# Optimization experiments

Measured on AMD Instinct MI355X. Metric: run time of the kernel, lower is better.

The kernel has to match this reference:

```python
import jax, jax.numpy as jnp
import numpy as np

N_NODES = 50000
N_EDGES = 800000
IN_DIM, HID_DIM, OUT_DIM = 128, 128, 64


def setup_inputs() -> dict:
    key = jax.random.key(0)
    ks = jax.random.split(key, 8)
    x = jax.random.normal(ks[0], (N_NODES, IN_DIM), dtype=jnp.float32)
    edge_index = jax.random.randint(ks[1], (2, N_EDGES), 0, N_NODES, dtype=jnp.int64)
    # GCNConv uses Glorot weights + zero bias; any random init is fine for a reference
    W1 = jax.random.normal(ks[2], (IN_DIM, HID_DIM), dtype=jnp.float32) / np.sqrt(IN_DIM)
    b1 = jnp.zeros((HID_DIM,), dtype=jnp.float32)
    W2 = jax.random.normal(ks[3], (HID_DIM, OUT_DIM), dtype=jnp.float32) / np.sqrt(HID_DIM)
    b2 = jnp.zeros((OUT_DIM,), dtype=jnp.float32)
    Wfc = jax.random.normal(ks[4], (OUT_DIM, 2), dtype=jnp.float32) / np.sqrt(OUT_DIM)
    bfc = jnp.zeros((2,), dtype=jnp.float32)
    return {"x": x, "edge_index": edge_index, "W1": W1, "b1": b1,
            "W2": W2, "b2": b2, "Wfc": Wfc, "bfc": bfc}


def _gcn_conv(x, src, dst, W, b, n_nodes):
    """PyG GCNConv: out = D^{-1/2} (A+I) D^{-1/2} (x W) + b."""
    xw = x @ W  # [N, F_out] transform before propagation
    ones = jnp.ones(src.shape[0], dtype=xw.dtype)
    deg = jax.ops.segment_sum(ones, dst, num_segments=n_nodes) + 1.0  # +1 for self-loop
    dinv = jax.lax.rsqrt(deg)
    norm = dinv[src] * dinv[dst]  # [E]
    msg = xw[src] * norm[:, None]  # gather + scale: [E, F_out]
    agg = jax.ops.segment_sum(msg, dst, num_segments=n_nodes)  # scatter-add
    agg = agg + xw * (dinv * dinv)[:, None]  # self-loop contribution (norm = 1/deg)
    return agg + b


def reference(x, edge_index, W1, b1, W2, b2, Wfc, bfc):
    n = x.shape[0]
    src, dst = edge_index[0], edge_index[1]
    h = jax.nn.relu(_gcn_conv(x, src, dst, W1, b1, n))
    # dropout is identity in eval mode
    h = _gcn_conv(h, src, dst, W2, b2, n)
    h = h @ Wfc + bfc
    return jax.nn.leaky_relu(h, negative_slope=0.01)
```

## Files before the change

kernel.cpp:

```cpp
#include <hip/hip_runtime.h>
#include <hip/hip_fp16.h>

#define IN_DIM 128
#define HID_DIM 128
#define OUT_DIM 64
#define BINW 128
#define BINSHIFT 7
#define MAXBIN 512
#define CAP 4096
#define CNTSTRIDE 16

__global__ __launch_bounds__(256) void k_scatter(const int* __restrict__ src,
                                                 const int* __restrict__ dst,
                                                 int* __restrict__ bin_cnt,
                                                 int* __restrict__ ovf_cnt,
                                                 unsigned int* __restrict__ ovf,
                                                 unsigned int* __restrict__ ebin,
                                                 int E, int nbin) {
    __shared__ int h[MAXBIN];
    __shared__ int base_s[MAXBIN];
    int t = threadIdx.x;
    for (int k = t; k < nbin; k += 256) h[k] = 0;
    __syncthreads();
    int per = E / gridDim.x;
    int ebeg = blockIdx.x * per;
    int eend = (blockIdx.x + 1 == gridDim.x) ? E : ebeg + per;
    for (int i = ebeg + t; i < eend; i += 256)
        atomicAdd(&h[dst[i] >> BINSHIFT], 1);
    __syncthreads();
    for (int k = t; k < nbin; k += 256) {
        int c = h[k];
        base_s[k] = (c > 0) ? atomicAdd(&bin_cnt[k * CNTSTRIDE], c) : 0;
        h[k] = 0;
    }
    __syncthreads();
    for (int i = ebeg + t; i < eend; i += 256) {
        unsigned int s = (unsigned int)src[i];
        unsigned int d = (unsigned int)dst[i];
        int b = (int)(d >> BINSHIFT);
        int pos = base_s[b] + atomicAdd(&h[b], 1);
        unsigned int packed = s | (d << 16);
        if (pos < CAP) ebin[(size_t)b * CAP + pos] = packed;
        else ovf[atomicAdd(ovf_cnt, 1)] = packed;
    }
}

__global__ __launch_bounds__(256) void k_fill(const unsigned int* __restrict__ ebin,
                                              const int* __restrict__ bin_cnt,
                                              const int* __restrict__ ovf_cnt,
                                              const unsigned int* __restrict__ ovf,
                                              int* __restrict__ row_ptr,
                                              unsigned short* __restrict__ degu,
                                              unsigned short* __restrict__ csr_src,
                                              float* __restrict__ dinv,
                                              const float* __restrict__ W2,
                                              const float* __restrict__ Wfc,
                                              const float* __restrict__ b2,
                                              const float* __restrict__ bfc,
                                              float* __restrict__ Wc,
                                              float* __restrict__ bc,
                                              int N, int nbin) {
    __shared__ int cnt[BINW];
    __shared__ int excl[BINW];
    __shared__ int start[BINW];
    int k = blockIdx.x;
    int node0 = k * BINW;
    int nn = min(BINW, N - node0);
    int t = threadIdx.x;
    if (t < BINW) cnt[t] = 0;
    __syncthreads();
    int cnt_k = min(bin_cnt[k * CNTSTRIDE], CAP);
    const unsigned int* seg = ebin + (size_t)k * CAP;
    for (int i = t; i < cnt_k; i += 256)
        atomicAdd(&cnt[(seg[i] >> 16) & (BINW - 1)], 1);
    int novf = *ovf_cnt;
    for (int i = t; i < novf; i += 256) {
        unsigned int e = ovf[i];
        if ((int)(e >> (16 + BINSHIFT)) == k)
            atomicAdd(&cnt[(e >> 16) & (BINW - 1)], 1);
    }
    __syncthreads();
    if (t < BINW) excl[t] = (t < nn) ? cnt[t] : 0;
    __syncthreads();
    for (int off = 1; off < BINW; off <<= 1) {
        int u = 0;
        if (t < BINW && t >= off) u = excl[t - off];
        __syncthreads();
        if (t < BINW) excl[t] += u;
        __syncthreads();
    }
    if (t < nn) {
        int deg = cnt[t];
        int e0 = k * CAP + excl[t] - deg;
        start[t] = e0;
        row_ptr[node0 + t] = e0;
        degu[node0 + t] = (unsigned short)deg;
        dinv[node0 + t] = rsqrtf((float)deg + 1.0f);
        cnt[t] = 0;
    }
    __syncthreads();
    for (int i = t; i < cnt_k; i += 256) {
        unsigned int e = seg[i];
        int dl = (e >> 16) & (BINW - 1);
        int slot = start[dl] + atomicAdd(&cnt[dl], 1);
        csr_src[slot] = (unsigned short)(e & 0xffffu);
    }
    for (int i = t; i < novf; i += 256) {
        unsigned int e = ovf[i];
        if ((int)(e >> (16 + BINSHIFT)) == k) {
            int dl = (e >> 16) & (BINW - 1);
            int slot = start[dl] + atomicAdd(&cnt[dl], 1);
            csr_src[slot] = (unsigned short)(e & 0xffffu);
        }
    }
    if (k == 0) {
        int kk = t >> 1, j = t & 1;
        float acc = 0.f;
#pragma unroll 8
        for (int m = 0; m < OUT_DIM; ++m) acc += W2[kk * OUT_DIM + m] * Wfc[m * 2 + j];
        Wc[kk * 2 + j] = acc;
        if (kk == 0) {
            float b = 0.f;
#pragma unroll 8
            for (int m = 0; m < OUT_DIM; ++m) b += b2[m] * Wfc[m * 2 + j];
            bc[j] = b + bfc[j];
        }
    }
}

__global__ __launch_bounds__(256) void k_gemm1(const float* __restrict__ x,
                                               const float* __restrict__ W,
                                               const float* __restrict__ dinv,
                                               __half* __restrict__ xwh, int N) {
    __shared__ float Ws[64][128];
    int tid = threadIdx.x;
    float4* Ws4 = (float4*)&Ws[0][0];
    int tx = tid & 15, ty = tid >> 4;
    int row0 = blockIdx.x * 128;
    int rows[8];
    const float* xr[8];
#pragma unroll
    for (int j = 0; j < 8; ++j) {
        int row = row0 + ty + 16 * j;
        rows[j] = row;
        if (row > N - 1) row = N - 1;
        xr[j] = x + (size_t)row * IN_DIM;
    }
    float4 aclo[8], achi[8];
#pragma unroll
    for (int j = 0; j < 8; ++j) {
        aclo[j] = make_float4(0.f, 0.f, 0.f, 0.f);
        achi[j] = make_float4(0.f, 0.f, 0.f, 0.f);
    }
#pragma unroll
    for (int ph = 0; ph < 2; ++ph) {
        const float4* W4 = (const float4*)(W + (size_t)ph * 64 * HID_DIM);
#pragma unroll
        for (int i = 0; i < 8; ++i) Ws4[tid + 256 * i] = W4[tid + 256 * i];
        __syncthreads();
#pragma unroll 2
        for (int k4 = 0; k4 < 16; ++k4) {
            float4 av[8];
#pragma unroll
            for (int j = 0; j < 8; ++j) av[j] = *(const float4*)(xr[j] + ph * 64 + k4 * 4);
#pragma unroll
            for (int kk = 0; kk < 4; ++kk) {
                float4 blo = *(const float4*)&Ws[k4 * 4 + kk][4 * tx];
                float4 bhi = *(const float4*)&Ws[k4 * 4 + kk][64 + 4 * tx];
#pragma unroll
                for (int j = 0; j < 8; ++j) {
                    float a = (kk == 0) ? av[j].x : (kk == 1) ? av[j].y : (kk == 2) ? av[j].z : av[j].w;
                    aclo[j].x += a * blo.x; aclo[j].y += a * blo.y;
                    aclo[j].z += a * blo.z; aclo[j].w += a * blo.w;
                    achi[j].x += a * bhi.x; achi[j].y += a * bhi.y;
                    achi[j].z += a * bhi.z; achi[j].w += a * bhi.w;
                }
            }
        }
        __syncthreads();
    }
#pragma unroll
    for (int j = 0; j < 8; ++j) {
        if (rows[j] < N) {
            float dd = dinv[rows[j]];
            union { __half2 h[2]; uint2 u; } lo, hi;
            lo.h[0] = __floats2half2_rn(aclo[j].x * dd, aclo[j].y * dd);
            lo.h[1] = __floats2half2_rn(aclo[j].z * dd, aclo[j].w * dd);
            hi.h[0] = __floats2half2_rn(achi[j].x * dd, achi[j].y * dd);
            hi.h[1] = __floats2half2_rn(achi[j].z * dd, achi[j].w * dd);
            uint2* p = (uint2*)(xwh + (size_t)rows[j] * HID_DIM);
            p[tx] = lo.u;
            p[16 + tx] = hi.u;
        }
    }
}

__global__ __launch_bounds__(256) void k_agg1z(const int* __restrict__ row_ptr,
                                               const unsigned short* __restrict__ degu,
                                               const unsigned short* __restrict__ csr_src,
                                               const float* __restrict__ dinv,
                                               const __half* __restrict__ xwh,
                                               const float* __restrict__ b1,
                                               const float* __restrict__ Wc,
                                               float* __restrict__ z, int N) {
    constexpr int F = HID_DIM;
    constexpr int L = F / 8;
    constexpr int EPW = 64 / L;
    __shared__ float Wcs[HID_DIM * 2];
    int tid = threadIdx.x;
    if (tid < 64) ((float4*)Wcs)[tid] = ((const float4*)Wc)[tid];
    __syncthreads();
    int node = (blockIdx.x * 256 + tid) >> 6;
    if (node >= N) return;
    int lane = tid & 63;
    int sub = lane / L;
    int c   = lane % L;
    int beg = row_ptr[node];
    int end = beg + degu[node];
    float dd = dinv[node];
    uint4 us = *(const uint4*)(xwh + (size_t)node * F + c * 8);
    float4 b1a = *(const float4*)(b1 + c * 8);
    float4 b1b = *(const float4*)(b1 + c * 8 + 4);
    float a0 = 0.f, a1 = 0.f, a2 = 0.f, a3 = 0.f;
    float a4 = 0.f, a5 = 0.f, a6 = 0.f, a7 = 0.f;
    auto acc = [&](uint4 u) {
        float2 v0 = __half22float2(*(__half2*)&u.x);
        float2 v1 = __half22float2(*(__half2*)&u.y);
        float2 v2 = __half22float2(*(__half2*)&u.z);
        float2 v3 = __half22float2(*(__half2*)&u.w);
        a0 += v0.x; a1 += v0.y; a2 += v1.x; a3 += v1.y;
        a4 += v2.x; a5 += v2.y; a6 += v3.x; a7 += v3.y;
    };
    int j = beg + sub;
    for (; j + 3 * EPW < end; j += 4 * EPW) {
        int s0 = csr_src[j];
        int s1 = csr_src[j + EPW];
        int s2 = csr_src[j + 2 * EPW];
        int s3 = csr_src[j + 3 * EPW];
        uint4 u0 = *(const uint4*)(xwh + (size_t)s0 * F + c * 8);
        uint4 u1 = *(const uint4*)(xwh + (size_t)s1 * F + c * 8);
        uint4 u2 = *(const uint4*)(xwh + (size_t)s2 * F + c * 8);
        uint4 u3 = *(const uint4*)(xwh + (size_t)s3 * F + c * 8);
        acc(u0); acc(u1); acc(u2); acc(u3);
    }
    for (; j < end; j += EPW) {
        int s = csr_src[j];
        acc(*(const uint4*)(xwh + (size_t)s * F + c * 8));
    }
#pragma unroll
    for (int off = L; off < 64; off <<= 1) {
        a0 += __shfl_xor(a0, off); a1 += __shfl_xor(a1, off);
        a2 += __shfl_xor(a2, off); a3 += __shfl_xor(a3, off);
        a4 += __shfl_xor(a4, off); a5 += __shfl_xor(a5, off);
        a6 += __shfl_xor(a6, off); a7 += __shfl_xor(a7, off);
    }
    float2 v0 = __half22float2(*(__half2*)&us.x);
    float2 v1 = __half22float2(*(__half2*)&us.y);
    float2 v2 = __half22float2(*(__half2*)&us.z);
    float2 v3 = __half22float2(*(__half2*)&us.w);
    float h[8];
    h[0] = fmaxf((a0 + v0.x) * dd + b1a.x, 0.f);
    h[1] = fmaxf((a1 + v0.y) * dd + b1a.y, 0.f);
    h[2] = fmaxf((a2 + v1.x) * dd + b1a.z, 0.f);
    h[3] = fmaxf((a3 + v1.y) * dd + b1a.w, 0.f);
    h[4] = fmaxf((a4 + v2.x) * dd + b1b.x, 0.f);
    h[5] = fmaxf((a5 + v2.y) * dd + b1b.y, 0.f);
    h[6] = fmaxf((a6 + v3.x) * dd + b1b.z, 0.f);
    h[7] = fmaxf((a7 + v3.y) * dd + b1b.w, 0.f);
    float o0 = 0.f, o1 = 0.f;
#pragma unroll
    for (int k = 0; k < 8; ++k) {
        o0 += h[k] * Wcs[(c * 8 + k) * 2 + 0];
        o1 += h[k] * Wcs[(c * 8 + k) * 2 + 1];
    }
#pragma unroll
    for (int off = 1; off < L; off <<= 1) {
        o0 += __shfl_xor(o0, off);
        o1 += __shfl_xor(o1, off);
    }
    if (lane == 0) {
        float2 r; r.x = o0 * dd; r.y = o1 * dd;
        *(float2*)(z + (size_t)node * 2) = r;
    }
}

__global__ __launch_bounds__(256) void k_agg2(const int* __restrict__ row_ptr,
                                              const unsigned short* __restrict__ degu,
                                              const unsigned short* __restrict__ csr_src,
                                              const float* __restrict__ dinv,
                                              const float* __restrict__ z,
                                              const float* __restrict__ bc,
                                              float* __restrict__ out, int N) {
    int tid = threadIdx.x;
    int gwave = (blockIdx.x * 256 + tid) >> 6;
    int lane = tid & 63;
    int grp = lane >> 3, li = lane & 7;
    int node = gwave * 8 + grp;
    if (node >= N) return;
    int beg = row_ptr[node];
    int end = beg + degu[node];
    float s0 = 0.f, s1 = 0.f;
    int j = beg + li;
    for (; j + 8 < end; j += 16) {
        int sa = csr_src[j];
        int sb = csr_src[j + 8];
        float2 za = *(const float2*)(z + (size_t)sa * 2);
        float2 zb = *(const float2*)(z + (size_t)sb * 2);
        s0 += za.x + zb.x; s1 += za.y + zb.y;
    }
    if (j < end) {
        int s = csr_src[j];
        float2 zv = *(const float2*)(z + (size_t)s * 2);
        s0 += zv.x; s1 += zv.y;
    }
#pragma unroll
    for (int off = 1; off < 8; off <<= 1) {
        s0 += __shfl_xor(s0, off);
        s1 += __shfl_xor(s1, off);
    }
    if (li == 0) {
        float2 zs = *(const float2*)(z + (size_t)node * 2);
        float dd = dinv[node];
        float o0 = (s0 + zs.x) * dd + bc[0];
        float o1 = (s1 + zs.y) * dd + bc[1];
        float2 r;
        r.x = o0 > 0.f ? o0 : 0.01f * o0;
        r.y = o1 > 0.f ? o1 : 0.01f * o1;
        *(float2*)(out + (size_t)node * 2) = r;
    }
}

extern "C" void kernel_launch(void* const* d_in, const int* in_sizes, int n_in,
                              void* d_out, int out_size, void* d_ws, size_t ws_size,
                              hipStream_t stream) {
    const float* x   = (const float*)d_in[0];
    const int*   ei  = (const int*)d_in[1];
    const float* W1  = (const float*)d_in[2];
    const float* b1  = (const float*)d_in[3];
    const float* W2  = (const float*)d_in[4];
    const float* b2  = (const float*)d_in[5];
    const float* Wfc = (const float*)d_in[6];
    const float* bfc = (const float*)d_in[7];

    const int N = in_sizes[0] / IN_DIM;
    const int E = in_sizes[1] / 2;
    const int* src = ei;
    const int* dst = ei + E;
    const int nbin = (N + BINW - 1) / BINW;

    char* base = (char*)d_ws;
    size_t off = 0;
    auto take = [&](size_t bytes) { size_t o = off; off = (off + bytes + 255) & ~(size_t)255; return (void*)(base + o); };
    int*    row_ptr  = (int*)take((size_t)N * 4);
    unsigned short* degu = (unsigned short*)take((size_t)N * 2);
    unsigned short* csr_src = (unsigned short*)take((size_t)nbin * CAP * 2);
    int*    bin_cnt  = (int*)take((size_t)(nbin * CNTSTRIDE + CNTSTRIDE) * 4);
    int*    ovf_cnt  = bin_cnt + nbin * CNTSTRIDE;
    unsigned int* ovf = (unsigned int*)take((size_t)E * 4);
    unsigned int* ebin = (unsigned int*)take((size_t)nbin * CAP * 4);
    float*  dinv     = (float*)take((size_t)N * 4);
    __half* xw1h     = (__half*)take((size_t)N * HID_DIM * 2);
    float*  zbuf     = (float*)take((size_t)N * 2 * 4);
    float*  Wc       = (float*)take((size_t)HID_DIM * 2 * 4);
    float*  bc       = (float*)take(2 * 4);

    hipMemsetAsync(bin_cnt, 0, (size_t)(nbin * CNTSTRIDE + CNTSTRIDE) * 4, stream);

    k_scatter<<<256, 256, 0, stream>>>(src, dst, bin_cnt, ovf_cnt, ovf, ebin, E, nbin);
    k_fill<<<nbin, 256, 0, stream>>>(ebin, bin_cnt, ovf_cnt, ovf, row_ptr, degu,
                                     csr_src, dinv, W2, Wfc, b2, bfc, Wc, bc, N, nbin);

    const int nTile = (N + 127) / 128;

    k_gemm1<<<nTile, 256, 0, stream>>>(x, W1, dinv, xw1h, N);
    k_agg1z<<<(N + 3) / 4, 256, 0, stream>>>(row_ptr, degu, csr_src, dinv, xw1h, b1, Wc, zbuf, N);
    const int nAgg2 = ((N + 7) / 8 * 64 + 255) / 256;
    k_agg2<<<nAgg2, 256, 0, stream>>>(row_ptr, degu, csr_src, dinv, zbuf, bc, (float*)d_out, N);
}
```

Measured before the change: 178.1 us.

## Split layer-1 aggregation into four 32-feature passes with slab layout

The GEMM now writes the half-precision hidden features as four column slabs of 32 features (each N x 32) instead of one row-major N x 128 array. The aggregation kernel runs one pass per slab, so each gather touches 64-byte rows and the working set of each pass (about 3.2 MB) fits in cache, with the four passes running as separate block ranges. The partial projections are summed and scaled by dinv in a new small kernel. In exchange, the CSR edge lists are read four times and there is an extra launch plus a partial-result buffer.

```diff
diff --git a/kernel.cpp b/kernel.cpp
--- a/kernel.cpp
+++ b/kernel.cpp
@@ -9,6 +9,8 @@
 #define MAXBIN 512
 #define CAP 4096
 #define CNTSTRIDE 16
+#define PDIM 32
+#define NPASS (HID_DIM / PDIM)
 
 __global__ __launch_bounds__(256) void k_scatter(const int* __restrict__ src,
                                                  const int* __restrict__ dst,
@@ -131,7 +133,7 @@
 __global__ __launch_bounds__(256) void k_gemm1(const float* __restrict__ x,
                                                const float* __restrict__ W,
                                                const float* __restrict__ dinv,
-                                               __half* __restrict__ xwh, int N) {
+                                               __half* __restrict__ xwp, int N) {
     __shared__ float Ws[64][128];
     int tid = threadIdx.x;
     float4* Ws4 = (float4*)&Ws[0][0];
@@ -179,6 +181,7 @@
         }
         __syncthreads();
     }
+    int plo = tx >> 3, c32 = 4 * (tx & 7);
 #pragma unroll
     for (int j = 0; j < 8; ++j) {
         if (rows[j] < N) {
@@ -188,39 +191,40 @@
             lo.h[1] = __floats2half2_rn(aclo[j].z * dd, aclo[j].w * dd);
             hi.h[0] = __floats2half2_rn(achi[j].x * dd, achi[j].y * dd);
             hi.h[1] = __floats2half2_rn(achi[j].z * dd, achi[j].w * dd);
-            uint2* p = (uint2*)(xwh + (size_t)rows[j] * HID_DIM);
-            p[tx] = lo.u;
-            p[16 + tx] = hi.u;
+            *(uint2*)(xwp + ((size_t)plo * N + rows[j]) * PDIM + c32) = lo.u;
+            *(uint2*)(xwp + ((size_t)(plo + 2) * N + rows[j]) * PDIM + c32) = hi.u;
         }
     }
 }
 
-__global__ __launch_bounds__(256) void k_agg1z(const int* __restrict__ row_ptr,
-                                               const unsigned short* __restrict__ degu,
-                                               const unsigned short* __restrict__ csr_src,
-                                               const float* __restrict__ dinv,
-                                               const __half* __restrict__ xwh,
-                                               const float* __restrict__ b1,
-                                               const float* __restrict__ Wc,
-                                               float* __restrict__ z, int N) {
-    constexpr int F = HID_DIM;
-    constexpr int L = F / 8;
-    constexpr int EPW = 64 / L;
+__global__ __launch_bounds__(256) void k_agg1zp(const int* __restrict__ row_ptr,
+                                                const unsigned short* __restrict__ degu,
+                                                const unsigned short* __restrict__ csr_src,
+                                                const float* __restrict__ dinv,
+                                                const __half* __restrict__ xwp,
+                                                const float* __restrict__ b1,
+                                                const float* __restrict__ Wc,
+                                                float* __restrict__ zp,
+                                                int N, int nodeBlocks) {
     __shared__ float Wcs[HID_DIM * 2];
     int tid = threadIdx.x;
     if (tid < 64) ((float4*)Wcs)[tid] = ((const float4*)Wc)[tid];
     __syncthreads();
-    int node = (blockIdx.x * 256 + tid) >> 6;
+    int pass = blockIdx.x / nodeBlocks;
+    int nb   = blockIdx.x % nodeBlocks;
+    int node = nb * 4 + (tid >> 6);
     if (node >= N) return;
     int lane = tid & 63;
-    int sub = lane / L;
-    int c   = lane % L;
+    int sub = lane >> 2;
+    int c   = lane & 3;
     int beg = row_ptr[node];
     int end = beg + degu[node];
+    const __half* xp = xwp + (size_t)pass * N * PDIM;
     float dd = dinv[node];
-    uint4 us = *(const uint4*)(xwh + (size_t)node * F + c * 8);
-    float4 b1a = *(const float4*)(b1 + c * 8);
-    float4 b1b = *(const float4*)(b1 + c * 8 + 4);
+    uint4 us = *(const uint4*)(xp + (size_t)node * PDIM + c * 8);
+    int d0 = pass * PDIM + c * 8;
+    float4 b1a = *(const float4*)(b1 + d0);
+    float4 b1b = *(const float4*)(b1 + d0 + 4);
     float a0 = 0.f, a1 = 0.f, a2 = 0.f, a3 = 0.f;
     float a4 = 0.f, a5 = 0.f, a6 = 0.f, a7 = 0.f;
     auto acc = [&](uint4 u) {
@@ -232,23 +236,19 @@
         a4 += v2.x; a5 += v2.y; a6 += v3.x; a7 += v3.y;
     };
     int j = beg + sub;
-    for (; j + 3 * EPW < end; j += 4 * EPW) {
+    for (; j + 16 < end; j += 32) {
         int s0 = csr_src[j];
-        int s1 = csr_src[j + EPW];
-        int s2 = csr_src[j + 2 * EPW];
-        int s3 = csr_src[j + 3 * EPW];
-        uint4 u0 = *(const uint4*)(xwh + (size_t)s0 * F + c * 8);
-        uint4 u1 = *(const uint4*)(xwh + (size_t)s1 * F + c * 8);
-        uint4 u2 = *(const uint4*)(xwh + (size_t)s2 * F + c * 8);
-        uint4 u3 = *(const uint4*)(xwh + (size_t)s3 * F + c * 8);
-        acc(u0); acc(u1); acc(u2); acc(u3);
-    }
-    for (; j < end; j += EPW) {
+        int s1 = csr_src[j + 16];
+        uint4 u0 = *(const uint4*)(xp + (size_t)s0 * PDIM + c * 8);
+        uint4 u1 = *(const uint4*)(xp + (size_t)s1 * PDIM + c * 8);
+        acc(u0); acc(u1);
+    }
+    if (j < end) {
         int s = csr_src[j];
-        acc(*(const uint4*)(xwh + (size_t)s * F + c * 8));
-    }
-#pragma unroll
-    for (int off = L; off < 64; off <<= 1) {
+        acc(*(const uint4*)(xp + (size_t)s * PDIM + c * 8));
+    }
+#pragma unroll
+    for (int off = 4; off < 64; off <<= 1) {
         a0 += __shfl_xor(a0, off); a1 += __shfl_xor(a1, off);
         a2 += __shfl_xor(a2, off); a3 += __shfl_xor(a3, off);
         a4 += __shfl_xor(a4, off); a5 += __shfl_xor(a5, off);
@@ -270,18 +270,31 @@
     float o0 = 0.f, o1 = 0.f;
 #pragma unroll
     for (int k = 0; k < 8; ++k) {
-        o0 += h[k] * Wcs[(c * 8 + k) * 2 + 0];
-        o1 += h[k] * Wcs[(c * 8 + k) * 2 + 1];
-    }
-#pragma unroll
-    for (int off = 1; off < L; off <<= 1) {
+        o0 += h[k] * Wcs[(d0 + k) * 2 + 0];
+        o1 += h[k] * Wcs[(d0 + k) * 2 + 1];
+    }
+#pragma unroll
+    for (int off = 1; off < 4; off <<= 1) {
         o0 += __shfl_xor(o0, off);
         o1 += __shfl_xor(o1, off);
     }
-    if (lane == 0) {
-        float2 r; r.x = o0 * dd; r.y = o1 * dd;
-        *(float2*)(z + (size_t)node * 2) = r;
-    }
+    if (lane == 0)
+        *(float2*)(zp + ((size_t)pass * N + node) * 2) = make_float2(o0, o1);
+}
+
+__global__ __launch_bounds__(256) void k_zsum(const float* __restrict__ zp,
+                                              const float* __restrict__ dinv,
+                                              float* __restrict__ z, int N) {
+    int t = blockIdx.x * 256 + threadIdx.x;
+    if (t >= N) return;
+    float2 s = make_float2(0.f, 0.f);
+#pragma unroll
+    for (int p = 0; p < NPASS; ++p) {
+        float2 v = *(const float2*)(zp + ((size_t)p * N + t) * 2);
+        s.x += v.x; s.y += v.y;
+    }
+    float dd = dinv[t];
+    *(float2*)(z + (size_t)t * 2) = make_float2(s.x * dd, s.y * dd);
 }
 
 __global__ __launch_bounds__(256) void k_agg2(const int* __restrict__ row_ptr,
@@ -359,7 +372,8 @@
     unsigned int* ovf = (unsigned int*)take((size_t)E * 4);
     unsigned int* ebin = (unsigned int*)take((size_t)nbin * CAP * 4);
     float*  dinv     = (float*)take((size_t)N * 4);
-    __half* xw1h     = (__half*)take((size_t)N * HID_DIM * 2);
+    __half* xwp      = (__half*)take((size_t)NPASS * N * PDIM * 2);
+    float*  zpart    = (float*)take((size_t)NPASS * N * 2 * 4);
     float*  zbuf     = (float*)take((size_t)N * 2 * 4);
     float*  Wc       = (float*)take((size_t)HID_DIM * 2 * 4);
     float*  bc       = (float*)take(2 * 4);
@@ -372,8 +386,11 @@
 
     const int nTile = (N + 127) / 128;
 
-    k_gemm1<<<nTile, 256, 0, stream>>>(x, W1, dinv, xw1h, N);
-    k_agg1z<<<(N + 3) / 4, 256, 0, stream>>>(row_ptr, degu, csr_src, dinv, xw1h, b1, Wc, zbuf, N);
+    k_gemm1<<<nTile, 256, 0, stream>>>(x, W1, dinv, xwp, N);
+    const int nodeBlocks = (N + 3) / 4;
+    k_agg1zp<<<NPASS * nodeBlocks, 256, 0, stream>>>(row_ptr, degu, csr_src, dinv,
+                                                     xwp, b1, Wc, zpart, N, nodeBlocks);
+    k_zsum<<<(N + 255) / 256, 256, 0, stream>>>(zpart, dinv, zbuf, N);
     const int nAgg2 = ((N + 7) / 8 * 64 + 255) / 256;
     k_agg2<<<nAgg2, 256, 0, stream>>>(row_ptr, degu, csr_src, dinv, zbuf, bc, (float*)d_out, N);
 }
```

After: 240.4 us. 1.35x slower.
